# Optimization experiments

Measured on AMD Instinct MI355X. Metric: run time of the kernel, lower is better.

The kernel has to match this reference:

```python
import jax, jax.numpy as jnp
import numpy as np

B, DIN, F, H, C = 8192, 2048, 2048, 2048, 345
EPS = 1e-5


def setup_inputs() -> dict:
    key = jax.random.key(0)
    ks = jax.random.split(key, 8)
    rng = np.random.default_rng(0)
    # labels and sort order (torch.sort is stable here via argsort kind='stable')
    y_np = rng.integers(0, C, size=B).astype(np.int64)
    order_np = np.argsort(y_np, kind='stable')
    ys = y_np[order_np]
    # per-class random permutations within each sorted segment (torch.randperm per interval)
    shuf1 = np.empty(B, dtype=np.int64)
    shuf2 = np.empty(B, dtype=np.int64)
    for c in np.unique(ys):
        idx = np.nonzero(ys == c)[0]
        shuf1[idx] = rng.permutation(idx)
        shuf2[idx] = rng.permutation(idx)
    s = 0.02  # weight init scale
    return {
        'x': jax.random.normal(ks[0], (B, DIN), jnp.float32),
        'lam': jnp.array([float(rng.beta(0.5, 0.5))], jnp.float32),
        'Wf': jax.random.normal(ks[1], (DIN, F), jnp.float32) * s,
        'bf': jnp.zeros((F,), jnp.float32),
        'W1': jax.random.normal(ks[2], (F, H), jnp.float32) * s,
        'b1': jnp.zeros((H,), jnp.float32),
        'g1': jnp.ones((H,), jnp.float32),
        'be1': jnp.zeros((H,), jnp.float32),
        'W2': jax.random.normal(ks[3], (H, H), jnp.float32) * s,
        'b2': jnp.zeros((H,), jnp.float32),
        'g2': jnp.ones((H,), jnp.float32),
        'be2': jnp.zeros((H,), jnp.float32),
        'W3': jax.random.normal(ks[4], (H, F), jnp.float32) * s,
        'b3': jnp.zeros((F,), jnp.float32),
        'g3': jnp.ones((F,), jnp.float32),
        'be3': jnp.zeros((F,), jnp.float32),
        'Wc': jax.random.normal(ks[5], (F, C), jnp.float32) * s,
        'bc': jnp.zeros((C,), jnp.float32),
        'y': jnp.asarray(y_np),
        'order': jnp.asarray(order_np),
        'shuf1': jnp.asarray(shuf1),
        'shuf2': jnp.asarray(shuf2),
    }


def _bn(x, g, b):
    # BatchNorm1d, training mode: biased batch stats
    m = jnp.mean(x, axis=0)
    v = jnp.var(x, axis=0)
    return (x - m) * jax.lax.rsqrt(v + EPS) * g + b


def reference(x, lam, Wf, bf, W1, b1, g1, be1, W2, b2, g2, be2, W3, b3, g3, be3, Wc, bc, y, order, shuf1, shuf2):
    lam = lam[0]
    xs = x[order]           # sorted-by-label gather (vectorized)
    ys = y[order]
    feat = jax.nn.relu(xs @ Wf + bf)                      # featurizer
    h = jax.nn.relu(_bn(feat @ W1 + b1, g1, be1))         # cdpl projector
    h = jax.nn.relu(_bn(h @ W2 + b2, g2, be2))
    proj = _bn(h @ W3 + b3, g3, be3)
    out = feat @ Wc + bc                                  # classifier logits
    out2, feat2 = out[shuf1], proj[shuf1]                 # per-class shuffles
    out3, feat3 = out[shuf2], proj[shuf2]
    out3 = lam * out2 + (1.0 - lam) * out3
    feat3 = lam * feat2 + (1.0 - lam) * feat3
    mse = lambda a, b: jnp.mean((a - b) ** 2)
    L_ind_logit = mse(out, out2)
    L_hdl_logit = mse(out, out3)
    L_ind_feat = 0.3 * mse(proj, feat2)
    L_hdl_feat = 0.3 * mse(proj, feat3)
    logp = jax.nn.log_softmax(out, axis=-1)
    cl_loss = -jnp.mean(jnp.take_along_axis(logp, ys[:, None], axis=-1))
    C_scale = jax.lax.stop_gradient(jnp.minimum(cl_loss, 1.0))  # .item() -> constant
    loss = cl_loss + C_scale * (lam * (L_ind_logit + L_ind_feat) + (1.0 - lam) * (L_hdl_logit + L_hdl_feat))
    return loss
```

## Files before the change

### kernel.cpp

```cpp
#include <hip/hip_runtime.h>

#define NB   8192
#define NF   2048
#define NC   345
#define NCP  384
#define EPSV 1e-5f

#define SX   (5.75f / 127.0f)
#define SW   (0.115f / 127.0f)
#define SF   (5.2f / 127.0f)
#define SH   (5.75f / 127.0f)
#define ST1  (3.34f / 127.0f)
#define ST2  (3.68f / 127.0f)
#define QX   (1.0f / SX)
#define QW   (1.0f / SW)
#define QF   (1.0f / SF)
#define QH   (1.0f / SH)
#define QT1  (1.0f / ST1)
#define QT2  (1.0f / ST2)

typedef __bf16 bf16x8 __attribute__((ext_vector_type(8)));
typedef float  f32x4  __attribute__((ext_vector_type(4)));
typedef int    i32x4  __attribute__((ext_vector_type(4)));

__device__ __forceinline__ float bs2f(unsigned int u) { return __uint_as_float(u << 16); }
__device__ __forceinline__ unsigned short f2bs(float f) {
    unsigned int u = __float_as_uint(f);
    u += 0x7fffu + ((u >> 16) & 1u);
    return (unsigned short)(u >> 16);
}
__device__ __forceinline__ int q8i(float v, float iq) {
    int t = __float2int_rn(v * iq);
    return t > 127 ? 127 : (t < -127 ? -127 : t);
}

#define GLD16(g, l)                                                                     \
    __builtin_amdgcn_global_load_lds((const __attribute__((address_space(1))) void*)(g),\
                                     (__attribute__((address_space(3))) void*)(l),      \
                                     16, 0, 0)

__global__ void k_gather(const float* __restrict__ x, const int* __restrict__ order,
                         char* __restrict__ xq) {
    const int row = blockIdx.x;
    const long src = order[row];
    const float4* xr = (const float4*)(x + src * 2048);
    float4 a = xr[threadIdx.x * 2 + 0];
    float4 b = xr[threadIdx.x * 2 + 1];
    unsigned int lo = (unsigned)(q8i(a.x, QX) & 255) | ((unsigned)(q8i(a.y, QX) & 255) << 8) |
                      ((unsigned)(q8i(a.z, QX) & 255) << 16) | ((unsigned)(q8i(a.w, QX) & 255) << 24);
    unsigned int hi = (unsigned)(q8i(b.x, QX) & 255) | ((unsigned)(q8i(b.y, QX) & 255) << 8) |
                      ((unsigned)(q8i(b.z, QX) & 255) << 16) | ((unsigned)(q8i(b.w, QX) & 255) << 24);
    uint2 o; o.x = lo; o.y = hi;
    ((uint2*)(xq + (long)row * 2048))[threadIdx.x] = o;
}

__global__ void k_transpose4(const float* __restrict__ W0, const float* __restrict__ W1,
                             const float* __restrict__ W2, const float* __restrict__ W3,
                             char* __restrict__ Wt) {
    __shared__ float tile[32][33];
    const float* Wz = (blockIdx.z == 0) ? W0 : (blockIdx.z == 1) ? W1
                     : (blockIdx.z == 2) ? W2 : W3;
    char* out = Wt + (size_t)blockIdx.z * 2048 * 2048;
    const int n0 = blockIdx.x * 32, k0 = blockIdx.y * 32;
    const int tx = threadIdx.x, ty = threadIdx.y;
    #pragma unroll
    for (int i = 0; i < 32; i += 8)
        tile[ty + i][tx] = Wz[(long)(k0 + ty + i) * 2048 + n0 + tx];
    __syncthreads();
    #pragma unroll
    for (int i = 0; i < 32; i += 8)
        out[(long)(n0 + ty + i) * 2048 + k0 + tx] = (char)q8i(tile[tx][ty + i], QW);
}

__global__ void k_transposeC(const float* __restrict__ W, char* __restrict__ Wt8,
                             const float* __restrict__ bc, float* __restrict__ bcp,
                             int K, int N, int Npad) {
    __shared__ float tile[32][33];
    const int n0 = blockIdx.x * 32, k0 = blockIdx.y * 32;
    const int tx = threadIdx.x, ty = threadIdx.y;
    if (blockIdx.x == 0 && blockIdx.y == 0) {
        const int idx = ty * 32 + tx;
        for (int i = idx; i < Npad; i += 256) bcp[i] = (i < N) ? bc[i] : 0.f;
    }
    #pragma unroll
    for (int i = 0; i < 32; i += 8) {
        int n = n0 + tx, k = k0 + ty + i;
        tile[ty + i][tx] = (n < N) ? W[(long)k * N + n] : 0.f;
    }
    __syncthreads();
    #pragma unroll
    for (int i = 0; i < 32; i += 8) {
        int n = n0 + ty + i, k = k0 + tx;
        if (n < Npad) Wt8[(long)n * K + k] = (char)q8i(tile[tx][ty + i], QW);
    }
}

#define BARX  do { asm volatile("" ::: "memory"); __builtin_amdgcn_s_barrier(); \
                   asm volatile("" ::: "memory"); } while (0)
#define LGKM0 asm volatile("s_waitcnt lgkmcnt(0)" ::: "memory")
#define VMW4  asm volatile("s_waitcnt vmcnt(4)" ::: "memory")
#define VMW0  asm volatile("s_waitcnt vmcnt(0)" ::: "memory")

#define RDX(u, AV, BV) do {                                                            \
    const char* A_ = &L[((u) & 3) * 32768];                                            \
    const char* B_ = A_ + 16384;                                                       \
    _Pragma("unroll") for (int m_ = 0; m_ < 8; m_++)                                   \
        AV[m_] = *(const i32x4*)&A_[(wm * 128 + m_ * 16 + frow) * 64 + slt];           \
    _Pragma("unroll") for (int n_ = 0; n_ < 4; n_++)                                   \
        BV[n_] = *(const i32x4*)&B_[(wn * 64 + n_ * 16 + frow) * 64 + slt];            \
} while (0)

#define MMX(AV, BV) do {                                                               \
    __builtin_amdgcn_s_setprio(1);                                                     \
    _Pragma("unroll") for (int n_ = 0; n_ < 4; n_++)                                   \
    _Pragma("unroll") for (int m_ = 0; m_ < 8; m_++)                                   \
        acc[m_][n_] = __builtin_amdgcn_mfma_i32_16x16x64_i8(BV[n_], AV[m_],            \
                                                            acc[m_][n_], 0, 0, 0);    \
    __builtin_amdgcn_s_setprio(0);                                                     \
} while (0)

template <int RELU, int STATS>
__global__ __launch_bounds__(512, 2) void k_gemmq(
    const char* __restrict__ A,
    const char* __restrict__ Bt,
    const float* __restrict__ bias,
    char* __restrict__ C8,
    float* __restrict__ stats,
    float S, float IQ, int N, int K) {
    __shared__ char L[4 * 32768];
    const int tid  = threadIdx.x;
    const int lane = tid & 63;
    const int wv   = tid >> 6;
    const int frow = lane & 15;
    const int kg   = lane >> 4;
    const int wm   = wv >> 2;
    const int wn   = wv & 3;
    const int slt  = (kg ^ ((frow >> 1) & 3)) * 16;

    const int id  = blockIdx.x;
    const int xcd = id & 7, kid = id >> 3;
    const int brow = (xcd * 4 + (kid & 3)) * 256;
    const int bcol = (kid >> 2) * 256;

    const char* pA[2];
    const char* pB[2];
    #pragma unroll
    for (int i = 0; i < 2; i++) {
        const int q = tid + i * 512;
        const int j = q >> 2;
        const int c = (q & 3) ^ ((j >> 1) & 3);
        pA[i] = A  + (long)(brow + j) * K + c * 16;
        pB[i] = Bt + (long)(bcol + j) * K + c * 16;
    }

    i32x4 acc[8][4];
    #pragma unroll
    for (int m = 0; m < 8; m++)
        #pragma unroll
        for (int n = 0; n < 4; n++)
            #pragma unroll
            for (int r = 0; r < 4; r++) acc[m][n][r] = 0;

    auto stage = [&](int s) {
        char* Lb = &L[(s & 3) * 32768];
        const int ko = s * 64;
        GLD16(pA[0] + ko, Lb + wv * 1024);
        GLD16(pA[1] + ko, Lb + 8192 + wv * 1024);
        GLD16(pB[0] + ko, Lb + 16384 + wv * 1024);
        GLD16(pB[1] + ko, Lb + 24576 + wv * 1024);
    };

    i32x4 avA[8], bvA[4], avB[8], bvB[4];

    stage(0); stage(1); stage(2);
    VMW4; BARX;
    RDX(0, avA, bvA);

    for (int i = 0; i < 14; i++) {
        const int t = i * 2;
        RDX(t + 1, avB, bvB); stage(t + 3); MMX(avA, bvA); VMW4; BARX;
        RDX(t + 2, avA, bvA); stage(t + 4); MMX(avB, bvB); VMW4; BARX;
    }
    RDX(29, avB, bvB); stage(31); MMX(avA, bvA); VMW4; BARX;
    RDX(30, avA, bvA); MMX(avB, bvB); VMW0; BARX;
    RDX(31, avB, bvB); MMX(avA, bvA);
    MMX(avB, bvB);

    LGKM0; BARX;
    unsigned short* Ls = (unsigned short*)L;
    const int cbase = bcol + wn * 64 + kg * 4;
    #pragma unroll
    for (int n = 0; n < 4; n++) {
        const int col = cbase + n * 16;
        const float4 bb = *(const float4*)&bias[col];
        float s0_ = 0.f, s1_ = 0.f, s2_ = 0.f, s3_ = 0.f;
        float q0_ = 0.f, q1_ = 0.f, q2_ = 0.f, q3_ = 0.f;
        const int s8 = wn * 16 + n * 4 + kg;
        const int p8 = s8 ^ frow;
        #pragma unroll
        for (int m = 0; m < 8; m++) {
            const int rloc = wm * 128 + m * 16 + frow;
            float v0 = (float)acc[m][n][0] * S + bb.x;
            float v1 = (float)acc[m][n][1] * S + bb.y;
            float v2 = (float)acc[m][n][2] * S + bb.z;
            float v3 = (float)acc[m][n][3] * S + bb.w;
            if (STATS) { s0_ += v0; q0_ += v0 * v0; s1_ += v1; q1_ += v1 * v1;
                         s2_ += v2; q2_ += v2 * v2; s3_ += v3; q3_ += v3 * v3; }
            if (RELU) { v0 = fmaxf(v0, 0.f); v1 = fmaxf(v1, 0.f);
                        v2 = fmaxf(v2, 0.f); v3 = fmaxf(v3, 0.f); }
            ushort4 st; st.x = f2bs(v0); st.y = f2bs(v1); st.z = f2bs(v2); st.w = f2bs(v3);
            *(ushort4*)&Ls[rloc * 256 + p8 * 4] = st;
        }
        if (STATS) {
            #pragma unroll
            for (int off = 1; off <= 8; off <<= 1) {
                s0_ += __shfl_xor(s0_, off); s1_ += __shfl_xor(s1_, off);
                s2_ += __shfl_xor(s2_, off); s3_ += __shfl_xor(s3_, off);
                q0_ += __shfl_xor(q0_, off); q1_ += __shfl_xor(q1_, off);
                q2_ += __shfl_xor(q2_, off); q3_ += __shfl_xor(q3_, off);
            }
            if (frow == 0) {
                atomicAdd(&stats[col + 0], s0_); atomicAdd(&stats[col + 1], s1_);
                atomicAdd(&stats[col + 2], s2_); atomicAdd(&stats[col + 3], s3_);
                atomicAdd(&stats[N + col + 0], q0_); atomicAdd(&stats[N + col + 1], q1_);
                atomicAdd(&stats[N + col + 2], q2_); atomicAdd(&stats[N + col + 3], q3_);
            }
        }
    }
    LGKM0; BARX;
    #pragma unroll
    for (int it = 0; it < 16; it++) {
        const int c  = tid + it * 512;
        const int r  = c >> 5;
        const int a  = c & 31;
        const int x  = r & 15;
        const int a2 = a ^ (x >> 1);
        uint4 v = *(const uint4*)&Ls[r * 256 + a2 * 8];
        if (x & 1) { unsigned tx_ = v.x, ty_ = v.y; v.x = v.z; v.y = v.w; v.z = tx_; v.w = ty_; }
        const long grow = brow + r;
        const int  gcol = bcol + a * 8;
        unsigned int us[8] = {v.x & 0xffffu, v.x >> 16, v.y & 0xffffu, v.y >> 16,
                              v.z & 0xffffu, v.z >> 16, v.w & 0xffffu, v.w >> 16};
        unsigned int b[8];
        #pragma unroll
        for (int j = 0; j < 8; j++) b[j] = (unsigned)(q8i(bs2f(us[j]), IQ) & 255);
        uint2 o;
        o.x = b[0] | (b[1] << 8) | (b[2] << 16) | (b[3] << 24);
        o.y = b[4] | (b[5] << 8) | (b[6] << 16) | (b[7] << 24);
        *(uint2*)&C8[grow * N + gcol] = o;
    }
}

__global__ __launch_bounds__(256) void k_gemmc(const char* __restrict__ A,
                                               const char* __restrict__ Bt,
                                               const float* __restrict__ bias,
                                               unsigned short* __restrict__ outP,
                                               float S, int K) {
    __shared__ char As[2][8192];
    __shared__ char Bs[2][8192];
    const int tid  = threadIdx.x;
    const int lane = tid & 63;
    const int wv   = tid >> 6;
    const int brow = blockIdx.x * 128;
    const int bcol = blockIdx.y * 128;
    const int kz   = blockIdx.z;
    const long k0  = (long)kz * 1024;
    const int wr   = (wv >> 1) * 64;
    const int wc   = (wv & 1) * 64;
    const int frow = lane & 15;
    const int kg   = lane >> 4;
    const int slt  = (kg ^ ((frow >> 1) & 3)) * 16;

    const char* pA[2];
    const char* pB[2];
    #pragma unroll
    for (int i = 0; i < 2; i++) {
        const int q = tid + i * 256;
        const int j = q >> 2;
        const int c = (q & 3) ^ ((j >> 1) & 3);
        pA[i] = A  + (long)(brow + j) * K + k0 + c * 16;
        pB[i] = Bt + (long)(bcol + j) * K + k0 + c * 16;
    }

    i32x4 acc[4][4];
    #pragma unroll
    for (int m = 0; m < 4; m++)
        #pragma unroll
        for (int n = 0; n < 4; n++)
            #pragma unroll
            for (int r = 0; r < 4; r++) acc[m][n][r] = 0;

    auto stage = [&](int t, int b) {
        GLD16(pA[0] + t * 64, As[b] + wv * 1024);
        GLD16(pA[1] + t * 64, As[b] + 4096 + wv * 1024);
        GLD16(pB[0] + t * 64, Bs[b] + wv * 1024);
        GLD16(pB[1] + t * 64, Bs[b] + 4096 + wv * 1024);
    };

    stage(0, 0);
    __syncthreads();
    for (int t = 0; t < 16; t++) {
        if (t < 15) stage(t + 1, (t + 1) & 1);
        const int b = t & 1;
        i32x4 av[4], bv[4];
        #pragma unroll
        for (int m = 0; m < 4; m++)
            av[m] = *(const i32x4*)&As[b][(wr + m * 16 + frow) * 64 + slt];
        #pragma unroll
        for (int n = 0; n < 4; n++)
            bv[n] = *(const i32x4*)&Bs[b][(wc + n * 16 + frow) * 64 + slt];
        #pragma unroll
        for (int m = 0; m < 4; m++)
            #pragma unroll
            for (int n = 0; n < 4; n++)
                acc[m][n] = __builtin_amdgcn_mfma_i32_16x16x64_i8(bv[n], av[m],
                                                                  acc[m][n], 0, 0, 0);
        __syncthreads();
    }
    const int r0 = brow + wr + frow;
    const int c0 = bcol + wc + kg * 4;
    unsigned short* oz = outP + (long)kz * NB * NCP;
    #pragma unroll
    for (int n = 0; n < 4; n++) {
        const int col = c0 + n * 16;
        float4 bb = {0.f, 0.f, 0.f, 0.f};
        if (kz == 0) bb = *(const float4*)&bias[col];
        #pragma unroll
        for (int m = 0; m < 4; m++) {
            const long row = r0 + m * 16;
            ushort4 st;
            st.x = f2bs((float)acc[m][n][0] * S + bb.x);
            st.y = f2bs((float)acc[m][n][1] * S + bb.y);
            st.z = f2bs((float)acc[m][n][2] * S + bb.z);
            st.w = f2bs((float)acc[m][n][3] * S + bb.w);
            *(ushort4*)&oz[row * NCP + col] = st;
        }
    }
}

__global__ void k_bnapplyq8(const char* __restrict__ t8, const float* __restrict__ sums,
                            const float* __restrict__ g, const float* __restrict__ be,
                            char* __restrict__ o8, float St, int ncols) {
    const long i  = ((long)blockIdx.x * blockDim.x + threadIdx.x) * 8;
    const int  c0 = (int)(i & (ncols - 1));
    float sc[8], sh[8];
    #pragma unroll
    for (int j = 0; j < 8; j++) {
        const int c = c0 + j;
        const float m   = sums[c] * (1.f / NB);
        const float var = sums[ncols + c] * (1.f / NB) - m * m;
        const float s   = rsqrtf(var + EPSV) * g[c];
        sc[j] = s * St;
        sh[j] = be[c] - m * s;
    }
    uint2 v = *(const uint2*)(t8 + i);
    unsigned int b[8];
    #pragma unroll
    for (int j = 0; j < 8; j++) {
        const unsigned int w = (j < 4) ? v.x : v.y;
        const int raw = (int)(signed char)((w >> ((j & 3) * 8)) & 0xffu);
        float val = (float)raw * sc[j] + sh[j];
        val = fmaxf(val, 0.f);
        b[j] = (unsigned)(q8i(val, QH) & 255);
    }
    uint2 o;
    o.x = b[0] | (b[1] << 8) | (b[2] << 16) | (b[3] << 24);
    o.y = b[4] | (b[5] << 8) | (b[6] << 16) | (b[7] << 24);
    *(uint2*)(o8 + i) = o;
}

__global__ __launch_bounds__(256) void k_logitloss(const unsigned short* __restrict__ outP,
                            const int* __restrict__ y,
                            const int* __restrict__ order, const int* __restrict__ s1,
                            const int* __restrict__ s2, const float* __restrict__ lamp,
                            float* __restrict__ acc) {
    const int lane = threadIdx.x & 63;
    const int wv   = threadIdx.x >> 6;
    const int wid  = blockIdx.x * 4 + wv;
    const int nw   = gridDim.x * 4;
    const float lam = lamp[0];
    const unsigned short* P1 = outP + (long)NB * NCP;
    float ce = 0.f, d1 = 0.f, d2 = 0.f;
    for (int i = wid; i < NB; i += nw) {
        const long r0 = (long)i * NCP;
        const long r2 = (long)s1[i] * NCP;
        const long r3 = (long)s2[i] * NCP;
        float v[6];
        float mx = -1e30f;
        #pragma unroll
        for (int j = 0; j < 6; j++) {
            const int c = lane + j * 64;
            if (c < NC) {
                const float a  = bs2f(outP[r0 + c]) + bs2f(P1[r0 + c]);
                const float b  = bs2f(outP[r2 + c]) + bs2f(P1[r2 + c]);
                const float cc = bs2f(outP[r3 + c]) + bs2f(P1[r3 + c]);
                const float mix = lam * b + (1.f - lam) * cc;
                v[j] = a;
                d1 += (a - b) * (a - b);
                d2 += (a - mix) * (a - mix);
                mx = fmaxf(mx, a);
            } else v[j] = -1e30f;
        }
        #pragma unroll
        for (int off = 32; off; off >>= 1) mx = fmaxf(mx, __shfl_xor(mx, off));
        float se = 0.f;
        #pragma unroll
        for (int j = 0; j < 6; j++) se += expf(v[j] - mx);
        #pragma unroll
        for (int off = 32; off; off >>= 1) se += __shfl_xor(se, off);
        if (lane == 0) {
            const int yv = y[order[i]];
            const float oy = bs2f(outP[r0 + yv]) + bs2f(P1[r0 + yv]);
            ce += mx + logf(se) - oy;
        }
    }
    #pragma unroll
    for (int off = 32; off; off >>= 1) {
        d1 += __shfl_xor(d1, off);
        d2 += __shfl_xor(d2, off);
    }
    __shared__ float red[4][3];
    if (lane == 0) { red[wv][0] = ce; red[wv][1] = d1; red[wv][2] = d2; }
    __syncthreads();
    if (threadIdx.x == 0) {
        atomicAdd(&acc[0], red[0][0] + red[1][0] + red[2][0] + red[3][0]);
        atomicAdd(&acc[1], red[0][1] + red[1][1] + red[2][1] + red[3][1]);
        atomicAdd(&acc[2], red[0][2] + red[1][2] + red[2][2] + red[3][2]);
    }
}

__global__ __launch_bounds__(256) void k_featloss(const char* __restrict__ t3q,
                           const float* __restrict__ sums,
                           const float* __restrict__ g, const float* __restrict__ be,
                           const int* __restrict__ s1,
                           const int* __restrict__ s2, const float* __restrict__ lamp,
                           float* __restrict__ acc) {
    const int t = threadIdx.x;
    const float lam = lamp[0];
    float sc[8], sh[8];
    #pragma unroll
    for (int j = 0; j < 8; j++) {
        const int c = t * 8 + j;
        const float m   = sums[c] * (1.f / NB);
        const float var = sums[NF + c] * (1.f / NB) - m * m;
        const float s   = rsqrtf(var + EPSV) * g[c];
        sc[j] = s * ST2;
        sh[j] = be[c] - m * s;
    }
    float d1 = 0.f, d2 = 0.f;
    for (int i = blockIdx.x; i < NB; i += gridDim.x) {
        uint2 a = ((const uint2*)(t3q + (long)i * NF))[t];
        uint2 b = ((const uint2*)(t3q + (long)s1[i] * NF))[t];
        uint2 c = ((const uint2*)(t3q + (long)s2[i] * NF))[t];
        #pragma unroll
        for (int j = 0; j < 8; j++) {
            const unsigned int wa = (j < 4) ? a.x : a.y;
            const unsigned int wb = (j < 4) ? b.x : b.y;
            const unsigned int wc_ = (j < 4) ? c.x : c.y;
            const int sh8 = (j & 3) * 8;
            float pa = (float)(int)(signed char)((wa >> sh8) & 0xffu) * sc[j] + sh[j];
            float pb = (float)(int)(signed char)((wb >> sh8) & 0xffu) * sc[j] + sh[j];
            float pc = (float)(int)(signed char)((wc_ >> sh8) & 0xffu) * sc[j] + sh[j];
            float mix = lam * pb + (1.f - lam) * pc;
            d1 += (pa - pb) * (pa - pb);
            d2 += (pa - mix) * (pa - mix);
        }
    }
    #pragma unroll
    for (int off = 32; off; off >>= 1) {
        d1 += __shfl_xor(d1, off);
        d2 += __shfl_xor(d2, off);
    }
    __shared__ float r1[4], r2[4];
    if ((t & 63) == 0) { r1[t >> 6] = d1; r2[t >> 6] = d2; }
    __syncthreads();
    if (t == 0) {
        atomicAdd(&acc[3], r1[0] + r1[1] + r1[2] + r1[3]);
        atomicAdd(&acc[4], r2[0] + r2[1] + r2[2] + r2[3]);
    }
}

__global__ void k_final(const float* __restrict__ acc, const float* __restrict__ lamp,
                        float* __restrict__ outp) {
    const float lam = lamp[0];
    const float cl  = acc[0] * (1.f / NB);
    const float Lil = acc[1] * (1.f / ((float)NB * NC));
    const float Lhl = acc[2] * (1.f / ((float)NB * NC));
    const float Lif = 0.3f * acc[3] * (1.f / ((float)NB * NF));
    const float Lhf = 0.3f * acc[4] * (1.f / ((float)NB * NF));
    const float Cs  = fminf(cl, 1.f);
    outp[0] = cl + Cs * (lam * (Lil + Lif) + (1.f - lam) * (Lhl + Lhf));
}

extern "C" void kernel_launch(void* const* d_in, const int* in_sizes, int n_in,
                              void* d_out, int out_size, void* d_ws, size_t ws_size,
                              hipStream_t stream) {
    const float* x   = (const float*)d_in[0];
    const float* lam = (const float*)d_in[1];
    const float* Wf  = (const float*)d_in[2];
    const float* bf_ = (const float*)d_in[3];
    const float* W1  = (const float*)d_in[4];
    const float* b1  = (const float*)d_in[5];
    const float* g1  = (const float*)d_in[6];
    const float* be1 = (const float*)d_in[7];
    const float* W2  = (const float*)d_in[8];
    const float* b2  = (const float*)d_in[9];
    const float* g2  = (const float*)d_in[10];
    const float* be2 = (const float*)d_in[11];
    const float* W3  = (const float*)d_in[12];
    const float* b3  = (const float*)d_in[13];
    const float* g3  = (const float*)d_in[14];
    const float* be3 = (const float*)d_in[15];
    const float* Wc  = (const float*)d_in[16];
    const float* bc  = (const float*)d_in[17];
    const int* y     = (const int*)d_in[18];
    const int* order = (const int*)d_in[19];
    const int* s1    = (const int*)d_in[20];
    const int* s2    = (const int*)d_in[21];
    float* outp = (float*)d_out;

    char* ws = (char*)d_ws;
    const size_t MB = 1024 * 1024;
    char*  R0  = ws;
    char*  R2  = ws + 16 * MB;
    char*  R3  = ws + 32 * MB;
    unsigned short* outP = (unsigned short*)(ws + 48 * MB);
    char*  WT  = ws + 60 * MB;
    char*  WCT8 = ws + 76 * MB;
    float* stats = (float*)(ws + 77 * MB);
    float* accs  = stats + 3 * 4096;
    float* bcp   = accs + 16;

    hipMemsetAsync(stats, 0, (3 * 4096 + 8) * sizeof(float), stream);

    dim3 tb(32, 8);
    k_transpose4<<<dim3(64, 64, 4), tb, 0, stream>>>(Wf, W1, W2, W3, WT);
    k_transposeC<<<dim3(12, 64), tb, 0, stream>>>(Wc, WCT8, bc, bcp, 2048, NC, NCP);

    k_gather<<<NB, 256, 0, stream>>>(x, order, R0);

    k_gemmq<1, 0><<<256, 512, 0, stream>>>(R0, WT, bf_, R2, nullptr,
                                           SX * SW, QF, 2048, 2048);
    k_gemmc<<<dim3(64, 3, 2), 256, 0, stream>>>(R2, WCT8, bcp, outP, SF * SW, 2048);
    k_gemmq<0, 1><<<256, 512, 0, stream>>>(R2, WT + 4 * MB, b1, R3, stats,
                                           SF * SW, QT1, 2048, 2048);
    k_bnapplyq8<<<8192, 256, 0, stream>>>(R3, stats, g1, be1, R0, ST1, 2048);
    k_gemmq<0, 1><<<256, 512, 0, stream>>>(R0, WT + 8 * MB, b2, R3, stats + 4096,
                                           SH * SW, QT2, 2048, 2048);
    k_bnapplyq8<<<8192, 256, 0, stream>>>(R3, stats + 4096, g2, be2, R2, ST2, 2048);
    k_gemmq<0, 1><<<256, 512, 0, stream>>>(R2, WT + 12 * MB, b3, R3, stats + 8192,
                                           SH * SW, QT2, 2048, 2048);

    k_logitloss<<<512, 256, 0, stream>>>(outP, y, order, s1, s2, lam, accs);
    k_featloss<<<512, 256, 0, stream>>>(R3, stats + 8192, g3, be3, s1, s2, lam, accs);
    k_final<<<1, 1, 0, stream>>>(accs, lam, outp);
}
```

Baseline: 301.0 us.

## Split classifier GEMM four ways over K and widen weight transpose tiles

The classifier int8 GEMM now splits K into four 512-wide chunks instead of two. This doubles the grid (64x3x4 blocks) to fill more compute units, and the logit-loss kernel sums four bf16 partial planes instead of two, so the workspace layout is shifted to make room. The weight transpose/quantize kernel now handles 32x128 tiles per block and writes packed 4-byte outputs instead of single bytes, aiming for better store coalescing. In exchange the loss kernel reads more partial-sum memory, and summing more bf16 partials adds a little rounding error.

```diff
diff --git a/kernel.cpp b/kernel.cpp
--- a/kernel.cpp
+++ b/kernel.cpp
@@ -54,22 +54,34 @@
     ((uint2*)(xq + (long)row * 2048))[threadIdx.x] = o;
 }
 
-__global__ void k_transpose4(const float* __restrict__ W0, const float* __restrict__ W1,
-                             const float* __restrict__ W2, const float* __restrict__ W3,
-                             char* __restrict__ Wt) {
-    __shared__ float tile[32][33];
+__global__ __launch_bounds__(256) void k_transpose4(
+        const float* __restrict__ W0, const float* __restrict__ W1,
+        const float* __restrict__ W2, const float* __restrict__ W3,
+        char* __restrict__ Wt) {
+    __shared__ float tile[32][133];
     const float* Wz = (blockIdx.z == 0) ? W0 : (blockIdx.z == 1) ? W1
                      : (blockIdx.z == 2) ? W2 : W3;
     char* out = Wt + (size_t)blockIdx.z * 2048 * 2048;
-    const int n0 = blockIdx.x * 32, k0 = blockIdx.y * 32;
-    const int tx = threadIdx.x, ty = threadIdx.y;
-    #pragma unroll
-    for (int i = 0; i < 32; i += 8)
-        tile[ty + i][tx] = Wz[(long)(k0 + ty + i) * 2048 + n0 + tx];
+    const int n0 = blockIdx.x * 32, k0 = blockIdx.y * 128;
+    const int t = threadIdx.x;
+    #pragma unroll
+    for (int i = 0; i < 16; i++) {
+        const int e = t + i * 256;
+        const int k = e >> 5, n = e & 31;
+        tile[n][k] = Wz[(long)(k0 + k) * 2048 + n0 + n];
+    }
     __syncthreads();
     #pragma unroll
-    for (int i = 0; i < 32; i += 8)
-        out[(long)(n0 + ty + i) * 2048 + k0 + tx] = (char)q8i(tile[tx][ty + i], QW);
+    for (int i = 0; i < 4; i++) {
+        const int e = t + i * 256;
+        const int n = e >> 5;
+        const int j = (e & 31) * 4;
+        unsigned int o = (unsigned)(q8i(tile[n][j + 0], QW) & 255)
+                       | ((unsigned)(q8i(tile[n][j + 1], QW) & 255) << 8)
+                       | ((unsigned)(q8i(tile[n][j + 2], QW) & 255) << 16)
+                       | ((unsigned)(q8i(tile[n][j + 3], QW) & 255) << 24);
+        *(unsigned int*)&out[(long)(n0 + n) * 2048 + k0 + j] = o;
+    }
 }
 
 __global__ void k_transposeC(const float* __restrict__ W, char* __restrict__ Wt8,
@@ -264,7 +276,7 @@
     const int brow = blockIdx.x * 128;
     const int bcol = blockIdx.y * 128;
     const int kz   = blockIdx.z;
-    const long k0  = (long)kz * 1024;
+    const long k0  = (long)kz * 512;
     const int wr   = (wv >> 1) * 64;
     const int wc   = (wv & 1) * 64;
     const int frow = lane & 15;
@@ -299,8 +311,8 @@
 
     stage(0, 0);
     __syncthreads();
-    for (int t = 0; t < 16; t++) {
-        if (t < 15) stage(t + 1, (t + 1) & 1);
+    for (int t = 0; t < 8; t++) {
+        if (t < 7) stage(t + 1, (t + 1) & 1);
         const int b = t & 1;
         i32x4 av[4], bv[4];
         #pragma unroll
@@ -379,7 +391,7 @@
     const int wid  = blockIdx.x * 4 + wv;
     const int nw   = gridDim.x * 4;
     const float lam = lamp[0];
-    const unsigned short* P1 = outP + (long)NB * NCP;
+    const long PS = (long)NB * NCP;
     float ce = 0.f, d1 = 0.f, d2 = 0.f;
     for (int i = wid; i < NB; i += nw) {
         const long r0 = (long)i * NCP;
@@ -391,9 +403,13 @@
         for (int j = 0; j < 6; j++) {
             const int c = lane + j * 64;
             if (c < NC) {
-                const float a  = bs2f(outP[r0 + c]) + bs2f(P1[r0 + c]);
-                const float b  = bs2f(outP[r2 + c]) + bs2f(P1[r2 + c]);
-                const float cc = bs2f(outP[r3 + c]) + bs2f(P1[r3 + c]);
+                float a = 0.f, b = 0.f, cc = 0.f;
+                #pragma unroll
+                for (int z = 0; z < 4; z++) {
+                    a  += bs2f(outP[z * PS + r0 + c]);
+                    b  += bs2f(outP[z * PS + r2 + c]);
+                    cc += bs2f(outP[z * PS + r3 + c]);
+                }
                 const float mix = lam * b + (1.f - lam) * cc;
                 v[j] = a;
                 d1 += (a - b) * (a - b);
@@ -410,7 +426,9 @@
         for (int off = 32; off; off >>= 1) se += __shfl_xor(se, off);
         if (lane == 0) {
             const int yv = y[order[i]];
-            const float oy = bs2f(outP[r0 + yv]) + bs2f(P1[r0 + yv]);
+            float oy = 0.f;
+            #pragma unroll
+            for (int z = 0; z < 4; z++) oy += bs2f(outP[z * PS + r0 + yv]);
             ce += mx + logf(se) - oy;
         }
     }
@@ -525,23 +543,22 @@
     char*  R2  = ws + 16 * MB;
     char*  R3  = ws + 32 * MB;
     unsigned short* outP = (unsigned short*)(ws + 48 * MB);
-    char*  WT  = ws + 60 * MB;
-    char*  WCT8 = ws + 76 * MB;
-    float* stats = (float*)(ws + 77 * MB);
+    char*  WT  = ws + 72 * MB;
+    char*  WCT8 = ws + 88 * MB;
+    float* stats = (float*)(ws + 89 * MB);
     float* accs  = stats + 3 * 4096;
     float* bcp   = accs + 16;
 
     hipMemsetAsync(stats, 0, (3 * 4096 + 8) * sizeof(float), stream);
 
-    dim3 tb(32, 8);
-    k_transpose4<<<dim3(64, 64, 4), tb, 0, stream>>>(Wf, W1, W2, W3, WT);
-    k_transposeC<<<dim3(12, 64), tb, 0, stream>>>(Wc, WCT8, bc, bcp, 2048, NC, NCP);
+    k_transpose4<<<dim3(64, 16, 4), 256, 0, stream>>>(Wf, W1, W2, W3, WT);
+    k_transposeC<<<dim3(12, 64), dim3(32, 8), 0, stream>>>(Wc, WCT8, bc, bcp, 2048, NC, NCP);
 
     k_gather<<<NB, 256, 0, stream>>>(x, order, R0);
 
     k_gemmq<1, 0><<<256, 512, 0, stream>>>(R0, WT, bf_, R2, nullptr,
                                            SX * SW, QF, 2048, 2048);
-    k_gemmc<<<dim3(64, 3, 2), 256, 0, stream>>>(R2, WCT8, bcp, outP, SF * SW, 2048);
+    k_gemmc<<<dim3(64, 3, 4), 256, 0, stream>>>(R2, WCT8, bcp, outP, SF * SW, 2048);
     k_gemmq<0, 1><<<256, 512, 0, stream>>>(R2, WT + 4 * MB, b1, R3, stats,
                                            SF * SW, QT1, 2048, 2048);
     k_bnapplyq8<<<8192, 256, 0, stream>>>(R3, stats, g1, be1, R0, ST1, 2048);
```

Result: no change. 304.9 us (+1.3%).
